# Kernel optimization log

Measured on AMD Instinct MI355X. Metric: run time of the kernel, lower is better.

## Reference

```python
import jax, jax.numpy as jnp
import numpy as np

CH = 1024
NH = 16
HD = CH // NH


def setup_inputs() -> dict:
    key = jax.random.key(0)
    k1, k2, k3 = jax.random.split(key, 3)
    x = jax.random.normal(k1, (8, 1024, CH), dtype=jnp.float32)
    # torch.nn.Linear weights are [out, in]; store as [in, out] for x @ W
    s = 1.0 / np.sqrt(CH)
    W_qkv = jax.random.uniform(k2, (CH, 3 * CH), dtype=jnp.float32, minval=-s, maxval=s)
    W_out = jax.random.uniform(k3, (CH, CH), dtype=jnp.float32, minval=-s, maxval=s)
    return {"x": x, "W_qkv": W_qkv, "W_out": W_out}


def reference(x, W_qkv, W_out):
    B, N, C = x.shape
    qkv = x @ W_qkv                                   # [B, N, 3C]
    q, k, v = jnp.split(qkv, 3, axis=-1)
    # [B, N, C] -> [B, H, N, D]
    def heads(t):
        return t.reshape(B, N, NH, HD).transpose(0, 2, 1, 3)
    q, k, v = heads(q), heads(k), heads(v)
    scale = 1.0 / np.sqrt(HD).astype(np.float32)
    scores = jnp.einsum('bhqd,bhkd->bhqk', q, k) * scale
    attn = jax.nn.softmax(scores, axis=-1)
    out = jnp.einsum('bhqk,bhkd->bhqd', attn, v)      # [B, H, N, D]
    out = out.transpose(0, 2, 1, 3).reshape(B, N, C)
    return out @ W_out
```

## Files before the change

kernel.cpp:

```cpp
#include <hip/hip_runtime.h>
#include <math.h>

#define NH 16
#define HD 64

typedef unsigned short u16;
typedef unsigned int   u32;
using bf16x8 = __attribute__((ext_vector_type(8))) short;
using f32x4  = __attribute__((ext_vector_type(4))) float;
using u16x8  = __attribute__((ext_vector_type(8))) unsigned short;
using u16x4  = __attribute__((ext_vector_type(4))) unsigned short;
using u32x2  = __attribute__((ext_vector_type(2))) unsigned int;

__device__ __forceinline__ u16 f2bf(float x) {
    u32 u = __float_as_uint(x);
    u32 r = (u + 0x7FFFu + ((u >> 16) & 1u)) >> 16;
    return (u16)r;
}
__device__ __forceinline__ float bf2f(u16 h) { return __uint_as_float(((u32)h) << 16); }

#define GLDS16(src, dst) __builtin_amdgcn_global_load_lds( \
    (const __attribute__((address_space(1))) void*)(src),  \
    (__attribute__((address_space(3))) void*)(dst), 16, 0, 0)

#define LDS_OFF(p) ((u32)(uintptr_t)(__attribute__((address_space(3))) void*)(p))
#define DSREAD(d, a) asm volatile("ds_read_b128 %0, %1" : "=v"(d) : "v"(a))

#define MEMFENCE asm volatile("" ::: "memory")
#define BARMID { MEMFENCE; __builtin_amdgcn_s_barrier(); \
                 asm volatile("s_waitcnt lgkmcnt(0)" ::: "memory"); \
                 __builtin_amdgcn_sched_barrier(0); }
#define BAREND { MEMFENCE; __builtin_amdgcn_s_barrier(); MEMFENCE; }
#define VMW(n) asm volatile("s_waitcnt vmcnt(" #n ")" ::: "memory")

__global__ __launch_bounds__(256) void convert_x(const float* __restrict__ x,
                                                 u16* __restrict__ xt) {
    int t = blockIdx.x * 256 + threadIdx.x;
    int m = t >> 7;
    int k = (t & 127) * 8;
    const float4* src = (const float4*)(x + (size_t)m * 1024 + k);
    float4 v0 = src[0], v1 = src[1];
    float vs[8] = {v0.x, v0.y, v0.z, v0.w, v1.x, v1.y, v1.z, v1.w};
    u16x8 hv;
    #pragma unroll
    for (int j = 0; j < 8; j++) hv[j] = f2bf(vs[j]);
    *(u16x8*)(xt + (size_t)m * 1024 + k) = hv;
}

__global__ __launch_bounds__(256) void conv_w(const float* __restrict__ W,
                                              u16* __restrict__ wqk,
                                              u16* __restrict__ wv) {
    __shared__ float Ts[32][33];
    const int N = 3072;
    int k0 = blockIdx.y * 32, n0 = blockIdx.x * 32;
    int t = threadIdx.x;
    int r = t >> 3, c4 = (t & 7) * 4;
    float4 v = *(const float4*)(W + (size_t)(k0 + r) * N + n0 + c4);
    Ts[r][c4] = v.x; Ts[r][c4 + 1] = v.y; Ts[r][c4 + 2] = v.z; Ts[r][c4 + 3] = v.w;
    __syncthreads();
    int nl = t >> 3, kl = (t & 7) * 4;
    u16x4 hv;
    #pragma unroll
    for (int j = 0; j < 4; j++) hv[j] = f2bf(Ts[kl + j][nl]);
    int col = n0 + nl;
    if (col < 2048) {
        *(u16x4*)&wqk[(size_t)col * 1024 + k0 + kl] = hv;
    } else {
        *(u16x4*)&wv[(size_t)(col - 2048) * 1024 + k0 + kl] = hv;
    }
}

__global__ __launch_bounds__(256) void conv_wout(const float* __restrict__ W,
                                                 u16* __restrict__ Wt) {
    __shared__ float Ts[32][33];
    const int N = 1024;
    int k0 = blockIdx.y * 32, n0 = blockIdx.x * 32;
    int t = threadIdx.x;
    int r = t >> 3, c4 = (t & 7) * 4;
    float4 v = *(const float4*)(W + (size_t)(k0 + r) * N + n0 + c4);
    Ts[r][c4] = v.x; Ts[r][c4 + 1] = v.y; Ts[r][c4 + 2] = v.z; Ts[r][c4 + 3] = v.w;
    __syncthreads();
    int nl = t >> 3, kl = (t & 7) * 4;
    u16x4 hv;
    #pragma unroll
    for (int j = 0; j < 4; j++) hv[j] = f2bf(Ts[kl + j][nl]);
    *(u16x4*)&Wt[(size_t)(n0 + nl) * 1024 + k0 + kl] = hv;
}

__global__ __launch_bounds__(512, 2)
void gemm_qk_8ph(const u16* __restrict__ A, const u16* __restrict__ Bt,
                 u16* __restrict__ Qh, u16* __restrict__ Kh,
                 int Kp, int nbx) {
    __shared__ char LDS[131072];
    char* ldsA = LDS;
    char* ldsB = LDS + 65536;
    const u32 ldsAoff = LDS_OFF(ldsA);
    const u32 ldsBoff = ldsAoff + 65536;

    const int tid = threadIdx.x, lane = tid & 63, w = tid >> 6;
    const int wr = w >> 2, wc = w & 3;
    const int l15 = lane & 15;
    const int khb = (lane >> 4) << 4;
    const int lswz = (l15 & 7) << 4;
    const int Kp2 = Kp * 2;

    const int cpx = (int)gridDim.x >> 3;
    const int wg  = ((int)blockIdx.x & 7) * cpx + ((int)blockIdx.x >> 3);
    const int m0 = (wg / nbx) * 256, n0 = (wg % nbx) * 256;

    const int tp = tid >> 3;
    const int sw = ((tid & 7) * 16) ^ ((tp & 7) << 4);
    const int nA = ((tp >> 5) << 6) + (tp & 31);

    const char* Agb = (const char*)A  + (size_t)m0 * Kp2;
    const char* Bgb = (const char*)Bt + (size_t)n0 * Kp2;

#define STAGE_A(t, h, buf) { \
    const char* s_ = Agb + (t) * 128 + ((h) * 64 + tp) * Kp2 + sw; \
    char* d_ = ldsA + (buf) * 32768 + (h) * 16384 + (w << 10); \
    GLDS16(s_, d_); GLDS16(s_ + (size_t)128 * Kp2, d_ + 8192); }
#define STAGE_B(t, h, buf) { \
    const char* s_ = Bgb + (t) * 128 + (nA + (h) * 32) * Kp2 + sw; \
    char* d_ = ldsB + (buf) * 32768 + (h) * 16384 + (w << 10); \
    GLDS16(s_, d_); GLDS16(s_ + (size_t)128 * Kp2, d_ + 8192); }

    bf16x8 Af[4][2], Bf[2][2];

#define LOADA(buf, mh) { \
    _Pragma("unroll") \
    for (int mi = 0; mi < 4; ++mi) { \
        u32 rb_ = ldsAoff + (buf) * 32768 + (mh) * 16384 \
                + (u32)((wr * 64 + mi * 16 + l15) * 128); \
        DSREAD(Af[mi][0], rb_ + (u32)((khb) ^ lswz)); \
        DSREAD(Af[mi][1], rb_ + (u32)((64 + khb) ^ lswz)); \
    } }
#define LOADB(buf, nh) { \
    _Pragma("unroll") \
    for (int ni = 0; ni < 2; ++ni) { \
        u32 rb_ = ldsBoff + (buf) * 32768 + (nh) * 16384 \
                + (u32)((wc * 32 + ni * 16 + l15) * 128); \
        DSREAD(Bf[ni][0], rb_ + (u32)((khb) ^ lswz)); \
        DSREAD(Bf[ni][1], rb_ + (u32)((64 + khb) ^ lswz)); \
    } }
#define MM(mh, nh) { \
    __builtin_amdgcn_s_setprio(1); \
    _Pragma("unroll") \
    for (int kk = 0; kk < 2; ++kk) \
        _Pragma("unroll") \
        for (int mi = 0; mi < 4; ++mi) \
            _Pragma("unroll") \
            for (int ni = 0; ni < 2; ++ni) \
                acc[(mh) * 4 + mi][(nh) * 2 + ni] = \
                    __builtin_amdgcn_mfma_f32_16x16x32_bf16( \
                        Af[mi][kk], Bf[ni][kk], acc[(mh) * 4 + mi][(nh) * 2 + ni], 0, 0, 0); \
    __builtin_amdgcn_s_setprio(0); }

    f32x4 acc[8][4];
    #pragma unroll
    for (int i = 0; i < 8; i++)
        #pragma unroll
        for (int j = 0; j < 4; j++)
            acc[i][j] = f32x4{0.f, 0.f, 0.f, 0.f};

    const int NT = Kp >> 6;
    const int NITER = NT / 2 - 1;

    STAGE_B(0, 0, 0); STAGE_A(0, 1, 0); STAGE_B(0, 1, 0); STAGE_A(0, 0, 0);
    STAGE_B(1, 0, 1); STAGE_A(1, 1, 1); STAGE_B(1, 1, 1);
    VMW(6);
    MEMFENCE; __builtin_amdgcn_s_barrier(); MEMFENCE;

    for (int it = 0; it < NITER; ++it) {
        const int t = 2 * it;
        LOADA(0, 0); LOADB(0, 0); STAGE_A(t + 1, 0, 1);
        BARMID; MM(0, 0); BAREND;
        LOADA(0, 1); STAGE_B(t + 2, 0, 0);
        BARMID; MM(1, 0); BAREND;
        LOADB(0, 1); STAGE_A(t + 2, 1, 0);
        BARMID; MM(1, 1); BAREND;
        LOADA(0, 0); STAGE_B(t + 2, 1, 0); VMW(6);
        BARMID; MM(0, 1); BAREND;
        LOADA(1, 0); LOADB(1, 0); STAGE_A(t + 2, 0, 0);
        BARMID; MM(0, 0); BAREND;
        LOADA(1, 1); STAGE_B(t + 3, 0, 1);
        BARMID; MM(1, 0); BAREND;
        LOADB(1, 1); STAGE_A(t + 3, 1, 1);
        BARMID; MM(1, 1); BAREND;
        LOADA(1, 0); STAGE_B(t + 3, 1, 1); VMW(6);
        BARMID; MM(0, 1); BAREND;
    }

    LOADA(0, 0); LOADB(0, 0); STAGE_A(NT - 1, 0, 1);
    BARMID; MM(0, 0); BAREND;
    LOADA(0, 1);
    BARMID; MM(1, 0); BAREND;
    LOADB(0, 1);
    BARMID; MM(1, 1); BAREND;
    LOADA(0, 0); VMW(0);
    BARMID; MM(0, 1); BAREND;
    LOADA(1, 0); LOADB(1, 0);
    BARMID; MM(0, 0); BAREND;
    LOADA(1, 1);
    BARMID; MM(1, 0); BAREND;
    LOADB(1, 1);
    BARMID; MM(1, 1); BAREND;
    LOADA(1, 0);
    BARMID; MM(0, 1); BAREND;

    const int sel = n0 >> 10;
    u16* dst = (sel == 0) ? Qh : Kh;
    const float sc = (sel == 0) ? 0.125f * 1.4426950408889634f : 1.0f;
    #pragma unroll
    for (int mh = 0; mh < 2; ++mh)
        #pragma unroll
        for (int mi = 0; mi < 4; ++mi)
            #pragma unroll
            for (int nh = 0; nh < 2; ++nh)
                #pragma unroll
                for (int ni = 0; ni < 2; ++ni) {
                    f32x4 a = acc[mh * 4 + mi][nh * 2 + ni];
                    int col = n0 + wc * 64 + nh * 32 + ni * 16 + l15;
                    int within = col & 1023;
                    int hh = within >> 6, d = within & 63;
                    int rowb = m0 + wr * 128 + mh * 64 + mi * 16 + (lane >> 4) * 4;
                    int bb = rowb >> 10, n = rowb & 1023;
                    size_t hn = (size_t)(bb * NH + hh) * 1024 + n;
                    #pragma unroll
                    for (int reg = 0; reg < 4; reg++)
                        dst[(hn + reg) * 64 + d] = f2bf(a[reg] * sc);
                }
#undef STAGE_A
#undef STAGE_B
#undef LOADA
#undef LOADB
#undef MM
}

template<int MODE>
__global__ __launch_bounds__(256, 2)
void gemm_bf16(const u16* __restrict__ A, int lda,
               const u16* __restrict__ Bt, int ldb, int Kloop,
               float* __restrict__ C, u16* __restrict__ Vtr, int N, int nbx) {
    __shared__ u16 As[128 * 64];
    __shared__ u16 Bs[128 * 64];
    const char* AsC = (const char*)As;
    const char* BsC = (const char*)Bs;

    const int t = threadIdx.x;
    const int lane = t & 63, w = t >> 6;

    const int cpx = (int)gridDim.x >> 3;
    const int wg  = (blockIdx.x & 7) * cpx + (blockIdx.x >> 3);
    const int m0 = (wg / nbx) * 128, n0 = (wg % nbx) * 128;

    const int l15 = lane & 15;
    const int g16 = (lane >> 4) << 4;
    const int swz = (l15 & 7) << 4;

    const char* srcA[4];
    const char* srcB[4];
    char* dstA[4];
    char* dstB[4];
    #pragma unroll
    for (int i = 0; i < 4; i++) {
        int s = (w * 4 + i) * 64 + lane;
        int row  = (s * 16) >> 7;
        int colb = (s * 16) & 127;
        int scol = colb ^ ((row & 7) << 4);
        srcA[i] = (const char*)A  + ((size_t)(m0 + row) * lda) * 2 + scol;
        srcB[i] = (const char*)Bt + ((size_t)(n0 + row) * ldb) * 2 + scol;
        dstA[i] = (char*)As + (w * 4 + i) * 1024;
        dstB[i] = (char*)Bs + (w * 4 + i) * 1024;
    }

    const int wm = (w >> 1) * 64, wn = (w & 1) * 64;
    int rA[4], rB[4];
    #pragma unroll
    for (int i = 0; i < 4; i++) {
        rA[i] = (wm + i * 16 + l15) * 128;
        rB[i] = (wn + i * 16 + l15) * 128;
    }

    f32x4 acc[4][4];
    #pragma unroll
    for (int i = 0; i < 4; i++)
        #pragma unroll
        for (int j = 0; j < 4; j++)
            acc[i][j] = f32x4{0.f, 0.f, 0.f, 0.f};

    for (int k0 = 0; k0 < Kloop; k0 += 64) {
        __syncthreads();
        #pragma unroll
        for (int i = 0; i < 4; i++) {
            GLDS16(srcA[i], dstA[i]);
            GLDS16(srcB[i], dstB[i]);
            srcA[i] += 128;
            srcB[i] += 128;
        }
        __syncthreads();
        #pragma unroll
        for (int kb = 0; kb < 2; kb++) {
            const int csw = ((kb << 6) | g16) ^ swz;
            bf16x8 af[4], bfr[4];
            #pragma unroll
            for (int mi = 0; mi < 4; mi++) af[mi]  = *(const bf16x8*)(AsC + rA[mi] + csw);
            #pragma unroll
            for (int ni = 0; ni < 4; ni++) bfr[ni] = *(const bf16x8*)(BsC + rB[ni] + csw);
            #pragma unroll
            for (int mi = 0; mi < 4; mi++)
                #pragma unroll
                for (int ni = 0; ni < 4; ni++)
                    acc[mi][ni] = __builtin_amdgcn_mfma_f32_16x16x32_bf16(
                        af[mi], bfr[ni], acc[mi][ni], 0, 0, 0);
        }
    }

    if (MODE == 0) {
        #pragma unroll
        for (int mi = 0; mi < 4; mi++) {
            int rowb = m0 + wm + mi * 16 + (lane >> 4) * 4;
            #pragma unroll
            for (int ni = 0; ni < 4; ni++) {
                int col = n0 + wn + ni * 16 + l15;
                #pragma unroll
                for (int reg = 0; reg < 4; reg++)
                    C[(size_t)(rowb + reg) * N + col] = acc[mi][ni][reg];
            }
        }
    } else {
        #pragma unroll
        for (int ni = 0; ni < 4; ni++) {
            int col = n0 + wn + ni * 16 + l15;
            int hh = col >> 6, d = col & 63;
            #pragma unroll
            for (int mi = 0; mi < 4; mi++) {
                int rowb = m0 + wm + mi * 16 + (lane >> 4) * 4;
                int bb = rowb >> 10, n = rowb & 1023;
                u16x4 vv;
                #pragma unroll
                for (int reg = 0; reg < 4; reg++)
                    vv[reg] = f2bf(acc[mi][ni][reg]);
                *(u16x4*)&Vtr[((size_t)(bb * NH + hh) * 64 + d) * 1024 + n] = vv;
            }
        }
    }
}

__global__ __launch_bounds__(256, 4)
void attn_mfma(const u16* __restrict__ Qh, const u16* __restrict__ Kh,
               const u16* __restrict__ Vt, u16* __restrict__ AO) {
    __shared__ u16 Ks[64 * 64];
    __shared__ u16 Vs[64 * 64];
    __shared__ u16 Ps[4][16 * 72];

    const int t = threadIdx.x, lane = t & 63, w = t >> 6;

    const int orig = blockIdx.x;
    const int xcd = orig & 7, slot = orig >> 3;
    const int head_lin = xcd * 16 + (slot >> 4);
    const int qt = slot & 15;
    const int b = head_lin >> 4, h = head_lin & 15;
    const size_t head = (size_t)head_lin;

    const char* Qg = (const char*)(Qh + head * 1024 * 64) + qt * 64 * 128;
    const char* Kg = (const char*)(Kh + head * 1024 * 64);
    const char* Vg = (const char*)(Vt + head * 64 * 1024);
    char* KsC = (char*)Ks;
    char* VsC = (char*)Vs;
    char* PsC = (char*)(&Ps[w][0]);

    const int l15 = lane & 15;
    const int g16 = (lane >> 4) << 4;
    const int g8  = (lane >> 4) << 3;

    #pragma unroll
    for (int i = 0; i < 2; i++) {
        int c = (w * 2 + i) * 64 + lane;
        int row = c >> 3, colb = (c & 7) * 16;
        int soff = colb ^ ((row & 7) << 4);
        GLDS16(Kg + row * 128 + soff, KsC + (w * 2 + i) * 1024);
        GLDS16(Vg + row * 2048 + soff, VsC + (w * 2 + i) * 1024);
    }

    const int qrow = w * 16 + l15;
    bf16x8 qf[2];
    #pragma unroll
    for (int kk = 0; kk < 2; kk++)
        qf[kk] = *(const bf16x8*)(Qg + qrow * 128 + kk * 64 + g16);

    int ksrcoff[2], kdst[2], vsrcoff[2], vdst[2];
    #pragma unroll
    for (int i = 0; i < 2; i++) {
        int c = i * 256 + t;
        int row = c >> 3, colb = (c & 7) * 16;
        ksrcoff[i] = c * 16;
        kdst[i]    = row * 128 + (colb ^ ((row & 7) << 4));
        vsrcoff[i] = row * 2048 + colb;
        vdst[i]    = row * 128 + (colb ^ ((row & 7) << 4));
    }

    float lp = 0.f;
    f32x4 acc_o[4];
    #pragma unroll
    for (int i = 0; i < 4; i++) acc_o[i] = f32x4{0.f, 0.f, 0.f, 0.f};

    __syncthreads();

    for (int kt = 0; kt < 16; kt++) {
        u16x8 kst[2], vst[2];
        if (kt < 15) {
            const char* ks = Kg + (kt + 1) * 8192;
            const char* vs = Vg + (kt + 1) * 128;
            #pragma unroll
            for (int i = 0; i < 2; i++) {
                kst[i] = *(const u16x8*)(ks + ksrcoff[i]);
                vst[i] = *(const u16x8*)(vs + vsrcoff[i]);
            }
        }

        f32x4 sacc[4];
        #pragma unroll
        for (int c = 0; c < 4; c++) sacc[c] = f32x4{0.f, 0.f, 0.f, 0.f};
        __builtin_amdgcn_s_setprio(1);
        #pragma unroll
        for (int kk = 0; kk < 2; kk++) {
            int csw = ((kk * 64) | g16) ^ ((l15 & 7) << 4);
            #pragma unroll
            for (int c = 0; c < 4; c++) {
                bf16x8 bk = *(const bf16x8*)(KsC + (c * 16 + l15) * 128 + csw);
                sacc[c] = __builtin_amdgcn_mfma_f32_16x16x32_bf16(bk, qf[kk], sacc[c], 0, 0, 0);
            }
        }
        __builtin_amdgcn_s_setprio(0);

        {
            char* pb = PsC + l15 * 144 + g8;
            #pragma unroll
            for (int c = 0; c < 4; c++) {
                float p0 = __builtin_amdgcn_exp2f(sacc[c][0]);
                float p1 = __builtin_amdgcn_exp2f(sacc[c][1]);
                float p2 = __builtin_amdgcn_exp2f(sacc[c][2]);
                float p3 = __builtin_amdgcn_exp2f(sacc[c][3]);
                lp += (p0 + p1) + (p2 + p3);
                u32 w0, w1;
                asm("v_cvt_pk_bf16_f32 %0, %1, %2" : "=v"(w0) : "v"(p0), "v"(p1));
                asm("v_cvt_pk_bf16_f32 %0, %1, %2" : "=v"(w1) : "v"(p2), "v"(p3));
                u16x4 pk = __builtin_bit_cast(u16x4, u32x2{w0, w1});
                *(u16x4*)(pb + c * 32) = pk;
            }
        }
        MEMFENCE;
        asm volatile("s_waitcnt lgkmcnt(0)" ::: "memory");
        __builtin_amdgcn_sched_barrier(0);

        __builtin_amdgcn_s_setprio(1);
        #pragma unroll
        for (int kb = 0; kb < 2; kb++) {
            bf16x8 ap = *(const bf16x8*)(PsC + l15 * 144 + kb * 64 + g16);
            #pragma unroll
            for (int c2 = 0; c2 < 4; c2++) {
                int vrow = c2 * 16 + l15;
                int voff = vrow * 128 + (((kb << 6) | g16) ^ ((vrow & 7) << 4));
                bf16x8 bv = *(const bf16x8*)(VsC + voff);
                acc_o[c2] = __builtin_amdgcn_mfma_f32_16x16x32_bf16(ap, bv, acc_o[c2], 0, 0, 0);
            }
        }
        __builtin_amdgcn_s_setprio(0);

        __syncthreads();
        if (kt < 15) {
            #pragma unroll
            for (int i = 0; i < 2; i++) {
                *(u16x8*)(KsC + kdst[i]) = kst[i];
                *(u16x8*)(VsC + vdst[i]) = vst[i];
            }
            __syncthreads();
        }
    }

    lp += __shfl_xor(lp, 16, 64);
    lp += __shfl_xor(lp, 32, 64);
    float linv[4];
    #pragma unroll
    for (int reg = 0; reg < 4; reg++)
        linv[reg] = 1.0f / __shfl(lp, ((lane >> 4) << 2) + reg, 64);

    #pragma unroll
    for (int c2 = 0; c2 < 4; c2++) {
        int col = h * 64 + c2 * 16 + l15;
        #pragma unroll
        for (int reg = 0; reg < 4; reg++) {
            int row = b * 1024 + qt * 64 + w * 16 + (lane >> 4) * 4 + reg;
            float v = acc_o[c2][reg] * linv[reg];
            AO[(size_t)row * 1024 + col] = f2bf(v);
        }
    }
}

extern "C" void kernel_launch(void* const* d_in, const int* in_sizes, int n_in,
                              void* d_out, int out_size, void* d_ws, size_t ws_size,
                              hipStream_t stream) {
    const float* x    = (const float*)d_in[0];
    const float* Wqkv = (const float*)d_in[1];
    const float* Wout = (const float*)d_in[2];
    float* out = (float*)d_out;

    u16* xt    = (u16*)d_ws;
    u16* wqk   = xt + 8192ull * 1024;
    u16* wv    = wqk + 2048ull * 1024;
    u16* woutt = wv + 1024ull * 1024;
    u16* Qh    = woutt + 1024ull * 1024;
    u16* Kh    = Qh + 128ull * 1024 * 64;
    u16* Vtr   = Kh + 128ull * 1024 * 64;
    u16* AO    = xt;

    convert_x<<<4096, 256, 0, stream>>>(x, xt);
    conv_w<<<dim3(96, 32), 256, 0, stream>>>(Wqkv, wqk, wv);
    conv_wout<<<dim3(32, 32), 256, 0, stream>>>(Wout, woutt);

    gemm_qk_8ph<<<256, 512, 0, stream>>>(xt, wqk, Qh, Kh, 1024, 8);

    gemm_bf16<2><<<512, 256, 0, stream>>>(
        xt, 1024, wv, 1024, 1024, nullptr, Vtr, 1024, 8);

    attn_mfma<<<2048, 256, 0, stream>>>(Qh, Kh, Vtr, AO);

    gemm_bf16<0><<<512, 256, 0, stream>>>(
        AO, 1024, woutt, 1024, 1024, out, nullptr, 1024, 8);
}
```

Measured before the change: 153.0 us.

## Process two query tiles per attention block to reuse K/V tiles

Result: faster. 146.0 us, median of 2 (-4.6%).

```diff
diff --git a/kernel.cpp b/kernel.cpp
--- a/kernel.cpp
+++ b/kernel.cpp
@@ -351,18 +351,18 @@
                const u16* __restrict__ Vt, u16* __restrict__ AO) {
     __shared__ u16 Ks[64 * 64];
     __shared__ u16 Vs[64 * 64];
-    __shared__ u16 Ps[4][16 * 72];
+    __shared__ u16 Ps[4][2 * 16 * 72];
 
     const int t = threadIdx.x, lane = t & 63, w = t >> 6;
 
     const int orig = blockIdx.x;
     const int xcd = orig & 7, slot = orig >> 3;
-    const int head_lin = xcd * 16 + (slot >> 4);
-    const int qt = slot & 15;
+    const int head_lin = xcd * 16 + (slot >> 3);
+    const int qt = slot & 7;
     const int b = head_lin >> 4, h = head_lin & 15;
     const size_t head = (size_t)head_lin;
 
-    const char* Qg = (const char*)(Qh + head * 1024 * 64) + qt * 64 * 128;
+    const char* Qg = (const char*)(Qh + head * 1024 * 64) + qt * 128 * 128;
     const char* Kg = (const char*)(Kh + head * 1024 * 64);
     const char* Vg = (const char*)(Vt + head * 64 * 1024);
     char* KsC = (char*)Ks;
@@ -383,10 +383,12 @@
     }
 
     const int qrow = w * 16 + l15;
-    bf16x8 qf[2];
-    #pragma unroll
-    for (int kk = 0; kk < 2; kk++)
-        qf[kk] = *(const bf16x8*)(Qg + qrow * 128 + kk * 64 + g16);
+    bf16x8 qf[2][2];
+    #pragma unroll
+    for (int qs = 0; qs < 2; qs++)
+        #pragma unroll
+        for (int kk = 0; kk < 2; kk++)
+            qf[qs][kk] = *(const bf16x8*)(Qg + (qs * 64 + qrow) * 128 + kk * 64 + g16);
 
     int ksrcoff[2], kdst[2], vsrcoff[2], vdst[2];
     #pragma unroll
@@ -399,10 +401,12 @@
         vdst[i]    = row * 128 + (colb ^ ((row & 7) << 4));
     }
 
-    float lp = 0.f;
-    f32x4 acc_o[4];
-    #pragma unroll
-    for (int i = 0; i < 4; i++) acc_o[i] = f32x4{0.f, 0.f, 0.f, 0.f};
+    float lp[2] = {0.f, 0.f};
+    f32x4 acc_o[2][4];
+    #pragma unroll
+    for (int qs = 0; qs < 2; qs++)
+        #pragma unroll
+        for (int i = 0; i < 4; i++) acc_o[qs][i] = f32x4{0.f, 0.f, 0.f, 0.f};
 
     __syncthreads();
 
@@ -418,30 +422,31 @@
             }
         }
 
-        f32x4 sacc[4];
-        #pragma unroll
-        for (int c = 0; c < 4; c++) sacc[c] = f32x4{0.f, 0.f, 0.f, 0.f};
-        __builtin_amdgcn_s_setprio(1);
-        #pragma unroll
-        for (int kk = 0; kk < 2; kk++) {
-            int csw = ((kk * 64) | g16) ^ ((l15 & 7) << 4);
-            #pragma unroll
-            for (int c = 0; c < 4; c++) {
-                bf16x8 bk = *(const bf16x8*)(KsC + (c * 16 + l15) * 128 + csw);
-                sacc[c] = __builtin_amdgcn_mfma_f32_16x16x32_bf16(bk, qf[kk], sacc[c], 0, 0, 0);
-            }
-        }
-        __builtin_amdgcn_s_setprio(0);
-
-        {
-            char* pb = PsC + l15 * 144 + g8;
+        #pragma unroll
+        for (int qs = 0; qs < 2; qs++) {
+            f32x4 sacc[4];
+            #pragma unroll
+            for (int c = 0; c < 4; c++) sacc[c] = f32x4{0.f, 0.f, 0.f, 0.f};
+            __builtin_amdgcn_s_setprio(1);
+            #pragma unroll
+            for (int kk = 0; kk < 2; kk++) {
+                int csw = ((kk * 64) | g16) ^ ((l15 & 7) << 4);
+                #pragma unroll
+                for (int c = 0; c < 4; c++) {
+                    bf16x8 bk = *(const bf16x8*)(KsC + (c * 16 + l15) * 128 + csw);
+                    sacc[c] = __builtin_amdgcn_mfma_f32_16x16x32_bf16(bk, qf[qs][kk], sacc[c], 0, 0, 0);
+                }
+            }
+            __builtin_amdgcn_s_setprio(0);
+
+            char* pb = PsC + qs * 2304 + l15 * 144 + g8;
             #pragma unroll
             for (int c = 0; c < 4; c++) {
                 float p0 = __builtin_amdgcn_exp2f(sacc[c][0]);
                 float p1 = __builtin_amdgcn_exp2f(sacc[c][1]);
                 float p2 = __builtin_amdgcn_exp2f(sacc[c][2]);
                 float p3 = __builtin_amdgcn_exp2f(sacc[c][3]);
-                lp += (p0 + p1) + (p2 + p3);
+                lp[qs] += (p0 + p1) + (p2 + p3);
                 u32 w0, w1;
                 asm("v_cvt_pk_bf16_f32 %0, %1, %2" : "=v"(w0) : "v"(p0), "v"(p1));
                 asm("v_cvt_pk_bf16_f32 %0, %1, %2" : "=v"(w1) : "v"(p2), "v"(p3));
@@ -456,13 +461,15 @@
         __builtin_amdgcn_s_setprio(1);
         #pragma unroll
         for (int kb = 0; kb < 2; kb++) {
-            bf16x8 ap = *(const bf16x8*)(PsC + l15 * 144 + kb * 64 + g16);
+            bf16x8 ap0 = *(const bf16x8*)(PsC + l15 * 144 + kb * 64 + g16);
+            bf16x8 ap1 = *(const bf16x8*)(PsC + 2304 + l15 * 144 + kb * 64 + g16);
             #pragma unroll
             for (int c2 = 0; c2 < 4; c2++) {
                 int vrow = c2 * 16 + l15;
                 int voff = vrow * 128 + (((kb << 6) | g16) ^ ((vrow & 7) << 4));
                 bf16x8 bv = *(const bf16x8*)(VsC + voff);
-                acc_o[c2] = __builtin_amdgcn_mfma_f32_16x16x32_bf16(ap, bv, acc_o[c2], 0, 0, 0);
+                acc_o[0][c2] = __builtin_amdgcn_mfma_f32_16x16x32_bf16(ap0, bv, acc_o[0][c2], 0, 0, 0);
+                acc_o[1][c2] = __builtin_amdgcn_mfma_f32_16x16x32_bf16(ap1, bv, acc_o[1][c2], 0, 0, 0);
             }
         }
         __builtin_amdgcn_s_setprio(0);
@@ -478,21 +485,25 @@
         }
     }
 
-    lp += __shfl_xor(lp, 16, 64);
-    lp += __shfl_xor(lp, 32, 64);
-    float linv[4];
-    #pragma unroll
-    for (int reg = 0; reg < 4; reg++)
-        linv[reg] = 1.0f / __shfl(lp, ((lane >> 4) << 2) + reg, 64);
-
-    #pragma unroll
-    for (int c2 = 0; c2 < 4; c2++) {
-        int col = h * 64 + c2 * 16 + l15;
-        #pragma unroll
-        for (int reg = 0; reg < 4; reg++) {
-            int row = b * 1024 + qt * 64 + w * 16 + (lane >> 4) * 4 + reg;
-            float v = acc_o[c2][reg] * linv[reg];
-            AO[(size_t)row * 1024 + col] = f2bf(v);
+    #pragma unroll
+    for (int qs = 0; qs < 2; qs++) {
+        float l = lp[qs];
+        l += __shfl_xor(l, 16, 64);
+        l += __shfl_xor(l, 32, 64);
+        float linv[4];
+        #pragma unroll
+        for (int reg = 0; reg < 4; reg++)
+            linv[reg] = 1.0f / __shfl(l, ((lane >> 4) << 2) + reg, 64);
+
+        #pragma unroll
+        for (int c2 = 0; c2 < 4; c2++) {
+            int col = h * 64 + c2 * 16 + l15;
+            #pragma unroll
+            for (int reg = 0; reg < 4; reg++) {
+                int row = b * 1024 + qt * 128 + qs * 64 + w * 16 + (lane >> 4) * 4 + reg;
+                float v = acc_o[qs][c2][reg] * linv[reg];
+                AO[(size_t)row * 1024 + col] = f2bf(v);
+            }
         }
     }
 }
@@ -523,7 +534,7 @@
     gemm_bf16<2><<<512, 256, 0, stream>>>(
         xt, 1024, wv, 1024, 1024, nullptr, Vtr, 1024, 8);
 
-    attn_mfma<<<2048, 256, 0, stream>>>(Qh, Kh, Vtr, AO);
+    attn_mfma<<<1024, 256, 0, stream>>>(Qh, Kh, Vtr, AO);
 
     gemm_bf16<0><<<512, 256, 0, stream>>>(
         AO, 1024, woutt, 1024, 1024, out, nullptr, 1024, 8);
```
